# Kernel optimization log

Hardware: AMD Instinct MI355X
Metric: run time of the kernel (lower is better)

Reference implementation:

```python
import jax, jax.numpy as jnp
import numpy as np

EPS = 1e-5
DN = ('NCHW', 'OIHW', 'NCHW')


def _conv(x, w):
    return jax.lax.conv_general_dilated(x, w, (1, 1), 'SAME', dimension_numbers=DN)


def _bn(x, g, b, m, v):
    # eval-mode batchnorm over channel axis 1
    inv = jax.lax.rsqrt(v + EPS)
    return (x - m[:, None, None]) * (g * inv)[:, None, None] + b[:, None, None]


def setup_inputs() -> dict:
    key = jax.random.key(0)
    ks = jax.random.split(key, 32)
    dim, mid, B, H, W = 256, 128, 4, 128, 128
    d = {}
    d['x'] = jax.random.normal(ks[0], (B, dim, H, W), dtype=jnp.float32)

    def bn_params(i, c):
        return (jax.random.uniform(ks[i], (c,), dtype=jnp.float32) + 0.5,
                jax.random.normal(ks[i + 1], (c,), dtype=jnp.float32) * 0.1,
                jax.random.normal(ks[i + 2], (c,), dtype=jnp.float32) * 0.1,
                jax.random.uniform(ks[i + 3], (c,), dtype=jnp.float32) + 0.5)

    d['w_p1'] = jax.random.normal(ks[1], (mid, dim, 3, 3), dtype=jnp.float32) * 0.02
    d['g_p1'], d['b_p1'], d['m_p1'], d['v_p1'] = bn_params(2, mid)
    d['w_p2'] = jax.random.normal(ks[6], (mid, dim, 3, 3), dtype=jnp.float32) * 0.02
    d['g_p2'], d['b_p2'], d['m_p2'], d['v_p2'] = bn_params(7, mid)
    d['w_c1'] = jax.random.normal(ks[11], (dim, mid, 3, 3), dtype=jnp.float32) * 0.02
    d['g_c1'], d['b_c1'], d['m_c1'], d['v_c1'] = bn_params(12, dim)
    d['w_c2'] = jax.random.normal(ks[16], (dim, dim, 1, 1), dtype=jnp.float32) * 0.02
    d['g_c2'], d['b_c2'], d['m_c2'], d['v_c2'] = bn_params(17, dim)
    d['w_p3'] = jax.random.normal(ks[21], (dim, dim, 3, 3), dtype=jnp.float32) * 0.02
    d['g_p3'], d['b_p3'], d['m_p3'], d['v_p3'] = bn_params(22, dim)
    return d


def reference(x,
              w_p1, g_p1, b_p1, m_p1, v_p1,
              w_p2, g_p2, b_p2, m_p2, v_p2,
              w_c1, g_c1, b_c1, m_c1, v_c1,
              w_c2, g_c2, b_c2, m_c2, v_c2,
              w_p3, g_p3, b_p3, m_p3, v_p3):
    # conv-bn-relu branches (dim -> 128)
    p1 = jax.nn.relu(_bn(_conv(x, w_p1), g_p1, b_p1, m_p1, v_p1))
    p2 = jax.nn.relu(_bn(_conv(x, w_p2), g_p2, b_p2, m_p2, v_p2))
    # corner pooling: 'top' = reverse cummax over H (axis 2),
    #                 'left' = reverse cummax over W (axis 3)
    cp1 = jax.lax.cummax(p1, axis=2, reverse=True)
    cp2 = jax.lax.cummax(p2, axis=3, reverse=True)
    bn1 = _bn(_conv(cp1 + cp2, w_c1), g_c1, b_c1, m_c1, v_c1)
    bn2 = _bn(_conv(x, w_c2), g_c2, b_c2, m_c2, v_c2)
    r = jax.nn.relu(bn1 + bn2)
    out = jax.nn.relu(_bn(_conv(r, w_p3), g_p3, b_p3, m_p3, v_p3))
    return out
```

## Files before the change

kernel.cpp:

```cpp
#include <hip/hip_runtime.h>
#include <math.h>

#define HH 128
#define WW 128
#define HWSZ (128*128)

typedef __attribute__((ext_vector_type(8))) short short8;
typedef __attribute__((ext_vector_type(4))) float float4v;

__device__ inline short f2bf(float f) {
  unsigned x = __float_as_uint(f);
  unsigned r = (x + 0x7fffu + ((x >> 16) & 1u)) >> 16;
  return (short)r;
}
__device__ inline float bf2f(unsigned short u) {
  return __uint_as_float(((unsigned)u) << 16);
}
__device__ inline int swz(int row, int g) {
  return row * 32 + ((g ^ ((row >> 1) & 3)) << 3);
}

__global__ __launch_bounds__(256) void prep1_kernel(
    const float* __restrict__ x, short* __restrict__ xbf,
    const float* __restrict__ w_p1, const float* __restrict__ g_p1, const float* __restrict__ v_p1,
    const float* __restrict__ w_p2, const float* __restrict__ g_p2, const float* __restrict__ v_p2,
    short* __restrict__ wb12) {
  __shared__ short tile[32 * 264];
  const int bid = blockIdx.x;
  const int t = threadIdx.x;
  if (bid < 512) {
    const int h = bid & 127, b = bid >> 7;
    for (int wc = 0; wc < 4; wc++) {
      const int w0 = wc * 32;
      __syncthreads();
      #pragma unroll
      for (int coi = 0; coi < 8; coi++) {
        int ci = coi * 32 + (t >> 3);
        int wq = t & 7;
        float4v f = *(const float4v*)&x[((size_t)b * 256 + ci) * HWSZ + h * WW + w0 + wq * 4];
        tile[(wq * 4 + 0) * 264 + ci] = f2bf(f.x);
        tile[(wq * 4 + 1) * 264 + ci] = f2bf(f.y);
        tile[(wq * 4 + 2) * 264 + ci] = f2bf(f.z);
        tile[(wq * 4 + 3) * 264 + ci] = f2bf(f.w);
      }
      __syncthreads();
      #pragma unroll
      for (int pass = 0; pass < 4; pass++) {
        int wl = pass * 8 + (t >> 5);
        int ci8 = (t & 31) * 8;
        short8 v = *(const short8*)&tile[wl * 264 + ci8];
        *(short8*)&xbf[(((size_t)b * HH + h) * WW + w0 + wl) * 256 + ci8] = v;
      }
    }
  } else {
    int e = (bid - 512) * 256 + t;
    if (e >= 589824) return;
    const float* w; const float* g; const float* v; int co_off;
    if (e < 294912) { w = w_p1; g = g_p1; v = v_p1; co_off = 0; }
    else { e -= 294912; w = w_p2; g = g_p2; v = v_p2; co_off = 128; }
    int t9 = e % 9;
    int ci = (e / 9) & 255;
    int co = e / (9 * 256);
    float s = g[co] * rsqrtf(v[co] + 1e-5f);
    wb12[((size_t)t9 * 256 + co_off + co) * 256 + ci] = f2bf(w[e] * s);
  }
}

__global__ __launch_bounds__(256) void prep2_kernel(
    const float* __restrict__ w_c1, const float* __restrict__ g_c1, const float* __restrict__ v_c1,
    const float* __restrict__ w_c2, const float* __restrict__ g_c2, const float* __restrict__ v_c2,
    short* __restrict__ wbc1, short* __restrict__ wbc2) {
  int e = blockIdx.x * 256 + threadIdx.x;
  if (e < 294912) {
    int t9 = e % 9;
    int ci = (e / 9) & 127;
    int co = e / (9 * 128);
    float s = g_c1[co] * rsqrtf(v_c1[co] + 1e-5f);
    wbc1[((size_t)t9 * 256 + co) * 128 + ci] = f2bf(w_c1[e] * s);
  } else if (e < 360448) {
    int e2 = e - 294912;
    int co = e2 >> 8;
    float s = g_c2[co] * rsqrtf(v_c2[co] + 1e-5f);
    wbc2[e2] = f2bf(w_c2[e2] * s);
  }
}

__global__ void wcvt3_kernel(const float* __restrict__ w, const float* __restrict__ g,
                             const float* __restrict__ v, short* __restrict__ out,
                             int Cin, int CoutW, int co_off) {
  int idx = blockIdx.x * blockDim.x + threadIdx.x;
  int total = CoutW * Cin * 9;
  if (idx >= total) return;
  int t  = idx % 9;
  int ci = (idx / 9) % Cin;
  int co = idx / (9 * Cin);
  float s = g[co] * rsqrtf(v[co] + 1e-5f);
  out[((size_t)t * 256 + co_off + co) * Cin + ci] = f2bf(w[idx] * s);
}

template<int CIN_A, bool PHASE_B, int SHIFT_MODE, bool SPLIT_OUT, bool OUT_F32>
__global__ __launch_bounds__(256, 2) void conv_mfma(
    const short* __restrict__ srcA, const short* __restrict__ xB,
    const short* __restrict__ wbA, const short* __restrict__ wbB,
    const float* __restrict__ g0, const float* __restrict__ b0,
    const float* __restrict__ m0, const float* __restrict__ v0,
    const float* __restrict__ g1, const float* __restrict__ b1,
    const float* __restrict__ m1, const float* __restrict__ v1,
    void* __restrict__ out0, void* __restrict__ out1)
{
  __shared__ short A_s[130 * 32];
  __shared__ short B_s[3 * 256 * 32];

  const int tid  = threadIdx.x;
  const int wave = tid >> 6;
  const int lane = tid & 63;
  const int wm = wave & 1;
  const int wn = wave >> 1;
  const int lr = lane & 15;
  const int lk = lane >> 4;

  const int h  = blockIdx.x & 127;
  const int b  = blockIdx.x >> 7;

  constexpr int ncA = CIN_A / 32;
  const int dystart = (h == 0) ? 1 : 0;
  const int dyend   = (h == HH - 1) ? 2 : 3;
  const int chunksA = (dyend - dystart) * ncA;
  const int total   = chunksA + (PHASE_B ? 8 : 0);

  float4v acc[4][8];
  #pragma unroll
  for (int i = 0; i < 4; i++)
    #pragma unroll
    for (int j = 0; j < 8; j++) acc[i][j] = (float4v)(0.0f);

  short8 rA[3], rB[12];
  const short* aRow = nullptr;
  const short* bBase = nullptr;
  bool curIsA = true;

  auto decode = [&](int t, const short*& ar, const short*& bb, bool& isA) {
    isA = (t < chunksA);
    if (isA) {
      int dy  = dystart + t / ncA;
      int ci0 = (t % ncA) * 32;
      ar = srcA + (((size_t)b * HH + (h + dy - 1)) * WW) * CIN_A + ci0;
      bb = wbA + ((size_t)(dy * 3) * 256) * CIN_A + ci0;
    } else {
      int ci0 = (t - chunksA) * 32;
      ar = xB + (((size_t)b * HH + h) * WW) * 256 + ci0;
      bb = wbB + ci0;
    }
  };

  auto loadRegs = [&](const short* ar, const short* bb, bool isA) {
    if (isA) {
      #pragma unroll
      for (int i = 0; i < 2; i++) {
        int idx = tid + i * 256;
        int w = (idx >> 2) - 1, q = idx & 3;
        rA[i] = ((unsigned)w < (unsigned)WW)
                  ? *(const short8*)(ar + (size_t)w * CIN_A + q * 8) : (short8)(0);
      }
      if (tid < 8) {
        int idx = tid + 512;
        int w = (idx >> 2) - 1, q = idx & 3;
        rA[2] = ((unsigned)w < (unsigned)WW)
                  ? *(const short8*)(ar + (size_t)w * CIN_A + q * 8) : (short8)(0);
      }
      #pragma unroll
      for (int i = 0; i < 12; i++) {
        int idx = tid + i * 256;
        int dx = idx >> 10, rem = idx & 1023;
        int co = rem >> 2, q = rem & 3;
        rB[i] = *(const short8*)(bb + (size_t)(dx * 256 + co) * CIN_A + q * 8);
      }
    } else {
      #pragma unroll
      for (int i = 0; i < 2; i++) {
        int idx = tid + i * 256;
        int wp = idx >> 2, q = idx & 3;
        rA[i] = *(const short8*)(ar + (size_t)wp * 256 + q * 8);
      }
      #pragma unroll
      for (int i = 0; i < 4; i++) {
        int idx = tid + i * 256;
        int co = idx >> 2, q = idx & 3;
        rB[i] = *(const short8*)(bb + (size_t)co * 256 + q * 8);
      }
    }
  };

  auto storeLDS = [&](bool isA) {
    if (isA) {
      #pragma unroll
      for (int i = 0; i < 2; i++) {
        int idx = tid + i * 256;
        *(short8*)&A_s[swz(idx >> 2, idx & 3)] = rA[i];
      }
      if (tid < 8) {
        int idx = tid + 512;
        *(short8*)&A_s[swz(idx >> 2, idx & 3)] = rA[2];
      }
      #pragma unroll
      for (int i = 0; i < 12; i++) {
        int idx = tid + i * 256;
        int dx = idx >> 10, rem = idx & 1023;
        *(short8*)&B_s[swz(dx * 256 + (rem >> 2), rem & 3)] = rB[i];
      }
    } else {
      #pragma unroll
      for (int i = 0; i < 2; i++) {
        int idx = tid + i * 256;
        *(short8*)&A_s[swz(idx >> 2, idx & 3)] = rA[i];
      }
      #pragma unroll
      for (int i = 0; i < 4; i++) {
        int idx = tid + i * 256;
        *(short8*)&B_s[swz(idx >> 2, idx & 3)] = rB[i];
      }
    }
  };

  decode(0, aRow, bBase, curIsA);
  loadRegs(aRow, bBase, curIsA);

  for (int t = 0; t < total; t++) {
    bool isA = curIsA;
    __syncthreads();
    storeLDS(isA);
    __syncthreads();
    if (t + 1 < total) {
      decode(t + 1, aRow, bBase, curIsA);
      loadRegs(aRow, bBase, curIsA);
    }
    const int ndx = isA ? 3 : 1;
    for (int dx = 0; dx < ndx; dx++) {
      short8 af[4];
      #pragma unroll
      for (int mi = 0; mi < 4; mi++)
        af[mi] = *(const short8*)&A_s[swz(wm * 64 + mi * 16 + lr + dx, lk)];
      #pragma unroll
      for (int ni = 0; ni < 8; ni++) {
        short8 bfr = *(const short8*)&B_s[swz(dx * 256 + wn * 128 + ni * 16 + lr, lk)];
        #pragma unroll
        for (int mi = 0; mi < 4; mi++)
          acc[mi][ni] = __builtin_amdgcn_mfma_f32_16x16x32_bf16(af[mi], bfr, acc[mi][ni], 0, 0, 0);
      }
    }
  }

  #pragma unroll
  for (int ni = 0; ni < 8; ni++) {
    int c = wn * 128 + ni * 16 + lr;
    float sh;
    if (SHIFT_MODE == 0) {
      float s = g0[c] * rsqrtf(v0[c] + 1e-5f);
      sh = b0[c] - m0[c] * s;
    } else if (SHIFT_MODE == 1) {
      int cc = c & 127;
      const float* gg = (c < 128) ? g0 : g1;
      const float* bb = (c < 128) ? b0 : b1;
      const float* mm = (c < 128) ? m0 : m1;
      const float* vv = (c < 128) ? v0 : v1;
      float s = gg[cc] * rsqrtf(vv[cc] + 1e-5f);
      sh = bb[cc] - mm[cc] * s;
    } else {
      float s0 = g0[c] * rsqrtf(v0[c] + 1e-5f);
      float s1 = g1[c] * rsqrtf(v1[c] + 1e-5f);
      sh = (b0[c] - m0[c] * s0) + (b1[c] - m1[c] * s1);
    }
    #pragma unroll
    for (int mi = 0; mi < 4; mi++) {
      int px = wm * 64 + mi * 16 + lk * 4;
      float4v v = acc[mi][ni];
      v.x = fmaxf(v.x + sh, 0.0f);
      v.y = fmaxf(v.y + sh, 0.0f);
      v.z = fmaxf(v.z + sh, 0.0f);
      v.w = fmaxf(v.w + sh, 0.0f);
      if (OUT_F32) {
        float* ob = (float*)out0;
        *(float4v*)(ob + ((size_t)b * 256 + c) * HWSZ + (size_t)h * WW + px) = v;
      } else if (SPLIT_OUT) {
        short* ob = (short*)((c < 128) ? out0 : out1);
        size_t base = (((size_t)b * HH + h) * WW + px) * 128 + (c & 127);
        ob[base      ] = f2bf(v.x);
        ob[base + 128 ] = f2bf(v.y);
        ob[base + 256 ] = f2bf(v.z);
        ob[base + 384 ] = f2bf(v.w);
      } else {
        short* ob = (short*)out0;
        size_t base = (((size_t)b * HH + h) * WW + px) * 256 + c;
        ob[base      ] = f2bf(v.x);
        ob[base + 256 ] = f2bf(v.y);
        ob[base + 512 ] = f2bf(v.z);
        ob[base + 768 ] = f2bf(v.w);
      }
    }
  }
}

__global__ __launch_bounds__(256) void colscan_kernel(unsigned* __restrict__ p) {
  __shared__ float sm[2][2][64];
  const int t = threadIdx.x;
  const int wl = t >> 7, seg = (t >> 6) & 1, cp = t & 63;
  const int w = blockIdx.x * 2 + wl;
  const int b = blockIdx.y;
  const size_t colbase = ((size_t)b * HH * WW + w) * 64 + cp;
  float m0 = -INFINITY, m1 = -INFINITY;
  unsigned r[64];
  if (seg) {
    #pragma unroll
    for (int i = 0; i < 64; i++) {
      int h = 127 - i;
      size_t idx = colbase + (size_t)h * (WW * 64);
      unsigned u = p[idx];
      m0 = fmaxf(m0, bf2f((unsigned short)(u & 0xffff)));
      m1 = fmaxf(m1, bf2f((unsigned short)(u >> 16)));
      p[idx] = ((unsigned)(unsigned short)f2bf(m1) << 16) | (unsigned short)f2bf(m0);
    }
    sm[wl][0][cp] = m0;
    sm[wl][1][cp] = m1;
  } else {
    #pragma unroll
    for (int i = 0; i < 64; i++) {
      int h = 63 - i;
      unsigned u = p[colbase + (size_t)h * (WW * 64)];
      m0 = fmaxf(m0, bf2f((unsigned short)(u & 0xffff)));
      m1 = fmaxf(m1, bf2f((unsigned short)(u >> 16)));
      r[i] = ((unsigned)(unsigned short)f2bf(m1) << 16) | (unsigned short)f2bf(m0);
    }
  }
  __syncthreads();
  if (!seg) {
    float b0 = sm[wl][0][cp], b1 = sm[wl][1][cp];
    #pragma unroll
    for (int i = 0; i < 64; i++) {
      int h = 63 - i;
      float f0 = fmaxf(bf2f((unsigned short)(r[i] & 0xffff)), b0);
      float f1 = fmaxf(bf2f((unsigned short)(r[i] >> 16)), b1);
      p[colbase + (size_t)h * (WW * 64)] =
          ((unsigned)(unsigned short)f2bf(f1) << 16) | (unsigned short)f2bf(f0);
    }
  }
}

__global__ __launch_bounds__(256) void rowscan_add_kernel(
    const short* __restrict__ p2, short* __restrict__ p1) {
  __shared__ short pl[128 * 128];
  const int tid = threadIdx.x;
  const int hb = blockIdx.x;
  const int b  = blockIdx.y;
  const size_t base = (((size_t)b * HH + hb) * WW) * 128;

  #pragma unroll
  for (int i = 0; i < 8; i++) {
    int idx = tid + i * 256;
    *(short8*)&pl[idx * 8] = *(const short8*)(p2 + base + (size_t)idx * 8);
  }
  __syncthreads();
  if (tid < 128) {
    float m = -INFINITY;
    for (int w = WW - 1; w >= 0; w--) {
      int a = w * 128 + tid;
      m = fmaxf(m, bf2f((unsigned short)pl[a]));
      pl[a] = (short)f2bf(m);
    }
  }
  __syncthreads();
  #pragma unroll
  for (int i = 0; i < 8; i++) {
    int idx = tid + i * 256;
    short8 sv = *(const short8*)&pl[idx * 8];
    short8 ov = *(const short8*)(p1 + base + (size_t)idx * 8);
    short8 rv;
    #pragma unroll
    for (int j = 0; j < 8; j++)
      rv[j] = f2bf(bf2f((unsigned short)sv[j]) + bf2f((unsigned short)ov[j]));
    *(short8*)(p1 + base + (size_t)idx * 8) = rv;
  }
}

extern "C" void kernel_launch(void* const* d_in, const int* in_sizes, int n_in,
                              void* d_out, int out_size, void* d_ws, size_t ws_size,
                              hipStream_t stream) {
  const float* x    = (const float*)d_in[0];
  const float* w_p1 = (const float*)d_in[1];
  const float* g_p1 = (const float*)d_in[2];
  const float* b_p1 = (const float*)d_in[3];
  const float* m_p1 = (const float*)d_in[4];
  const float* v_p1 = (const float*)d_in[5];
  const float* w_p2 = (const float*)d_in[6];
  const float* g_p2 = (const float*)d_in[7];
  const float* b_p2 = (const float*)d_in[8];
  const float* m_p2 = (const float*)d_in[9];
  const float* v_p2 = (const float*)d_in[10];
  const float* w_c1 = (const float*)d_in[11];
  const float* g_c1 = (const float*)d_in[12];
  const float* b_c1 = (const float*)d_in[13];
  const float* m_c1 = (const float*)d_in[14];
  const float* v_c1 = (const float*)d_in[15];
  const float* w_c2 = (const float*)d_in[16];
  const float* g_c2 = (const float*)d_in[17];
  const float* b_c2 = (const float*)d_in[18];
  const float* m_c2 = (const float*)d_in[19];
  const float* v_c2 = (const float*)d_in[20];
  const float* w_p3 = (const float*)d_in[21];
  const float* g_p3 = (const float*)d_in[22];
  const float* b_p3 = (const float*)d_in[23];
  const float* m_p3 = (const float*)d_in[24];
  const float* v_p3 = (const float*)d_in[25];

  char* ws = (char*)d_ws;
  short* p1  = (short*)(ws + 0);
  short* p2  = (short*)(ws + 16777216);
  short* r   = (short*)(ws + 33554432);
  short* xbf = (short*)(ws + 67108864);
  short* wb12 = r;
  short* wbc1 = p2;
  short* wbc2 = (short*)(ws + 16777216 + 589824);
  short* wbp3 = p1;

  prep1_kernel<<<dim3(2816), 256, 0, stream>>>(x, xbf,
      w_p1, g_p1, v_p1, w_p2, g_p2, v_p2, wb12);

  conv_mfma<256, false, 1, true, false><<<dim3(512), 256, 0, stream>>>(
      xbf, nullptr, wb12, nullptr,
      g_p1, b_p1, m_p1, v_p1, g_p2, b_p2, m_p2, v_p2, (void*)p1, (void*)p2);

  colscan_kernel<<<dim3(64, 4), 256, 0, stream>>>((unsigned*)p1);
  rowscan_add_kernel<<<dim3(128, 4), 256, 0, stream>>>(p2, p1);

  prep2_kernel<<<dim3(1408), 256, 0, stream>>>(
      w_c1, g_c1, v_c1, w_c2, g_c2, v_c2, wbc1, wbc2);

  conv_mfma<128, true, 2, false, false><<<dim3(512), 256, 0, stream>>>(
      p1, xbf, wbc1, wbc2,
      g_c1, b_c1, m_c1, v_c1, g_c2, b_c2, m_c2, v_c2, (void*)r, nullptr);

  wcvt3_kernel<<<(256 * 256 * 9 + 255) / 256, 256, 0, stream>>>(w_p3, g_p3, v_p3, wbp3, 256, 256, 0);

  conv_mfma<256, false, 0, false, true><<<dim3(512), 256, 0, stream>>>(
      r, nullptr, wbp3, nullptr,
      g_p3, b_p3, m_p3, v_p3, nullptr, nullptr, nullptr, nullptr, d_out, nullptr);
}
```

Before: 416.0 us.

## Parallelize corner-pool scans into segments and merge p3 weight prep into prep2

The column scan now uses four 32-row segments per column instead of two 64-row halves, and the row scan splits each row into two 64-wide halves with a carry-max fixup. Both give more parallelism and shorter serial chains. The separate p3 weight conversion kernel is folded into prep2 and writes to a dedicated workspace region, so it no longer aliases p1. This removes one launch at the cost of a larger prep2 grid and extra shared-memory combine steps.

```diff
diff --git a/kernel.cpp b/kernel.cpp
--- a/kernel.cpp
+++ b/kernel.cpp
@@ -69,7 +69,8 @@
 __global__ __launch_bounds__(256) void prep2_kernel(
     const float* __restrict__ w_c1, const float* __restrict__ g_c1, const float* __restrict__ v_c1,
     const float* __restrict__ w_c2, const float* __restrict__ g_c2, const float* __restrict__ v_c2,
-    short* __restrict__ wbc1, short* __restrict__ wbc2) {
+    const float* __restrict__ w_p3, const float* __restrict__ g_p3, const float* __restrict__ v_p3,
+    short* __restrict__ wbc1, short* __restrict__ wbc2, short* __restrict__ wbp3) {
   int e = blockIdx.x * 256 + threadIdx.x;
   if (e < 294912) {
     int t9 = e % 9;
@@ -82,20 +83,14 @@
     int co = e2 >> 8;
     float s = g_c2[co] * rsqrtf(v_c2[co] + 1e-5f);
     wbc2[e2] = f2bf(w_c2[e2] * s);
-  }
-}
-
-__global__ void wcvt3_kernel(const float* __restrict__ w, const float* __restrict__ g,
-                             const float* __restrict__ v, short* __restrict__ out,
-                             int Cin, int CoutW, int co_off) {
-  int idx = blockIdx.x * blockDim.x + threadIdx.x;
-  int total = CoutW * Cin * 9;
-  if (idx >= total) return;
-  int t  = idx % 9;
-  int ci = (idx / 9) % Cin;
-  int co = idx / (9 * Cin);
-  float s = g[co] * rsqrtf(v[co] + 1e-5f);
-  out[((size_t)t * 256 + co_off + co) * Cin + ci] = f2bf(w[idx] * s);
+  } else if (e < 950272) {
+    int e3 = e - 360448;
+    int t9 = e3 % 9;
+    int ci = (e3 / 9) & 255;
+    int co = e3 / (9 * 256);
+    float s = g_p3[co] * rsqrtf(v_p3[co] + 1e-5f);
+    wbp3[((size_t)t9 * 256 + co) * 256 + ci] = f2bf(w_p3[e3] * s);
+  }
 }
 
 template<int CIN_A, bool PHASE_B, int SHIFT_MODE, bool SPLIT_OUT, bool OUT_F32>
@@ -301,53 +296,48 @@
 }
 
 __global__ __launch_bounds__(256) void colscan_kernel(unsigned* __restrict__ p) {
-  __shared__ float sm[2][2][64];
+  __shared__ float sm[4][2][64];
   const int t = threadIdx.x;
-  const int wl = t >> 7, seg = (t >> 6) & 1, cp = t & 63;
-  const int w = blockIdx.x * 2 + wl;
+  const int seg = t >> 6, cp = t & 63;
+  const int w = blockIdx.x;
   const int b = blockIdx.y;
   const size_t colbase = ((size_t)b * HH * WW + w) * 64 + cp;
   float m0 = -INFINITY, m1 = -INFINITY;
-  unsigned r[64];
-  if (seg) {
-    #pragma unroll
-    for (int i = 0; i < 64; i++) {
-      int h = 127 - i;
-      size_t idx = colbase + (size_t)h * (WW * 64);
-      unsigned u = p[idx];
-      m0 = fmaxf(m0, bf2f((unsigned short)(u & 0xffff)));
-      m1 = fmaxf(m1, bf2f((unsigned short)(u >> 16)));
-      p[idx] = ((unsigned)(unsigned short)f2bf(m1) << 16) | (unsigned short)f2bf(m0);
-    }
-    sm[wl][0][cp] = m0;
-    sm[wl][1][cp] = m1;
-  } else {
-    #pragma unroll
-    for (int i = 0; i < 64; i++) {
-      int h = 63 - i;
-      unsigned u = p[colbase + (size_t)h * (WW * 64)];
-      m0 = fmaxf(m0, bf2f((unsigned short)(u & 0xffff)));
-      m1 = fmaxf(m1, bf2f((unsigned short)(u >> 16)));
-      r[i] = ((unsigned)(unsigned short)f2bf(m1) << 16) | (unsigned short)f2bf(m0);
-    }
-  }
+  unsigned r[32];
+  const int htop = seg * 32 + 31;
+  #pragma unroll
+  for (int i = 0; i < 32; i++) {
+    int h = htop - i;
+    unsigned u = p[colbase + (size_t)h * (WW * 64)];
+    m0 = fmaxf(m0, bf2f((unsigned short)(u & 0xffff)));
+    m1 = fmaxf(m1, bf2f((unsigned short)(u >> 16)));
+    r[i] = ((unsigned)(unsigned short)f2bf(m1) << 16) | (unsigned short)f2bf(m0);
+  }
+  sm[seg][0][cp] = m0;
+  sm[seg][1][cp] = m1;
   __syncthreads();
-  if (!seg) {
-    float b0 = sm[wl][0][cp], b1 = sm[wl][1][cp];
-    #pragma unroll
-    for (int i = 0; i < 64; i++) {
-      int h = 63 - i;
-      float f0 = fmaxf(bf2f((unsigned short)(r[i] & 0xffff)), b0);
-      float f1 = fmaxf(bf2f((unsigned short)(r[i] >> 16)), b1);
-      p[colbase + (size_t)h * (WW * 64)] =
-          ((unsigned)(unsigned short)f2bf(f1) << 16) | (unsigned short)f2bf(f0);
-    }
+  float s0 = -INFINITY, s1 = -INFINITY;
+  #pragma unroll
+  for (int s = 0; s < 3; s++) {
+    if (seg + 1 + s < 4) {
+      s0 = fmaxf(s0, sm[seg + 1 + s][0][cp]);
+      s1 = fmaxf(s1, sm[seg + 1 + s][1][cp]);
+    }
+  }
+  #pragma unroll
+  for (int i = 0; i < 32; i++) {
+    int h = htop - i;
+    float f0 = fmaxf(bf2f((unsigned short)(r[i] & 0xffff)), s0);
+    float f1 = fmaxf(bf2f((unsigned short)(r[i] >> 16)), s1);
+    p[colbase + (size_t)h * (WW * 64)] =
+        ((unsigned)(unsigned short)f2bf(f1) << 16) | (unsigned short)f2bf(f0);
   }
 }
 
 __global__ __launch_bounds__(256) void rowscan_add_kernel(
     const short* __restrict__ p2, short* __restrict__ p1) {
   __shared__ short pl[128 * 128];
+  __shared__ float bm[128];
   const int tid = threadIdx.x;
   const int hb = blockIdx.x;
   const int b  = blockIdx.y;
@@ -359,24 +349,37 @@
     *(short8*)&pl[idx * 8] = *(const short8*)(p2 + base + (size_t)idx * 8);
   }
   __syncthreads();
-  if (tid < 128) {
+  {
+    const int seg = tid >> 7;
+    const int c = tid & 127;
     float m = -INFINITY;
-    for (int w = WW - 1; w >= 0; w--) {
-      int a = w * 128 + tid;
+    const int wtop = seg * 64 + 63;
+    for (int i = 0; i < 64; i++) {
+      int a = (wtop - i) * 128 + c;
       m = fmaxf(m, bf2f((unsigned short)pl[a]));
       pl[a] = (short)f2bf(m);
     }
+    if (seg) bm[c] = m;
   }
   __syncthreads();
   #pragma unroll
   for (int i = 0; i < 8; i++) {
     int idx = tid + i * 256;
+    int w = idx >> 4;
     short8 sv = *(const short8*)&pl[idx * 8];
     short8 ov = *(const short8*)(p1 + base + (size_t)idx * 8);
     short8 rv;
-    #pragma unroll
-    for (int j = 0; j < 8; j++)
-      rv[j] = f2bf(bf2f((unsigned short)sv[j]) + bf2f((unsigned short)ov[j]));
+    if (w < 64) {
+      #pragma unroll
+      for (int j = 0; j < 8; j++) {
+        float f = fmaxf(bf2f((unsigned short)sv[j]), bm[(idx & 15) * 8 + j]);
+        rv[j] = f2bf(f + bf2f((unsigned short)ov[j]));
+      }
+    } else {
+      #pragma unroll
+      for (int j = 0; j < 8; j++)
+        rv[j] = f2bf(bf2f((unsigned short)sv[j]) + bf2f((unsigned short)ov[j]));
+    }
     *(short8*)(p1 + base + (size_t)idx * 8) = rv;
   }
 }
@@ -419,7 +422,7 @@
   short* wb12 = r;
   short* wbc1 = p2;
   short* wbc2 = (short*)(ws + 16777216 + 589824);
-  short* wbp3 = p1;
+  short* wbp3 = (short*)(ws + 16777216 + 589824 + 131072);
 
   prep1_kernel<<<dim3(2816), 256, 0, stream>>>(x, xbf,
       w_p1, g_p1, v_p1, w_p2, g_p2, v_p2, wb12);
@@ -428,18 +431,16 @@
       xbf, nullptr, wb12, nullptr,
       g_p1, b_p1, m_p1, v_p1, g_p2, b_p2, m_p2, v_p2, (void*)p1, (void*)p2);
 
-  colscan_kernel<<<dim3(64, 4), 256, 0, stream>>>((unsigned*)p1);
+  colscan_kernel<<<dim3(128, 4), 256, 0, stream>>>((unsigned*)p1);
   rowscan_add_kernel<<<dim3(128, 4), 256, 0, stream>>>(p2, p1);
 
-  prep2_kernel<<<dim3(1408), 256, 0, stream>>>(
-      w_c1, g_c1, v_c1, w_c2, g_c2, v_c2, wbc1, wbc2);
+  prep2_kernel<<<dim3(3712), 256, 0, stream>>>(
+      w_c1, g_c1, v_c1, w_c2, g_c2, v_c2, w_p3, g_p3, v_p3, wbc1, wbc2, wbp3);
 
   conv_mfma<128, true, 2, false, false><<<dim3(512), 256, 0, stream>>>(
       p1, xbf, wbc1, wbc2,
       g_c1, b_c1, m_c1, v_c1, g_c2, b_c2, m_c2, v_c2, (void*)r, nullptr);
 
-  wcvt3_kernel<<<(256 * 256 * 9 + 255) / 256, 256, 0, stream>>>(w_p3, g_p3, v_p3, wbp3, 256, 256, 0);
-
   conv_mfma<256, false, 0, false, true><<<dim3(512), 256, 0, stream>>>(
       r, nullptr, wbp3, nullptr,
       g_p3, b_p3, m_p3, v_p3, nullptr, nullptr, nullptr, nullptr, d_out, nullptr);
```

Result: faster. 405.7 us (-2.5%).
